# Kernel tuning notes

Measured on AMD Instinct MI355X. Metric: run time of the kernel, lower is better.

The kernel has to match this reference:

```python
import jax, jax.numpy as jnp
import numpy as np

B, S, H, C = 16, 64, 1024, 16


def setup_inputs() -> dict:
    key = jax.random.key(0)
    ks = jax.random.split(key, 14)
    sH = 1.0 / np.sqrt(H)
    # binary strictly-lower-triangular ancestor mask (DAG adjacency)
    dep = (jax.random.uniform(ks[0], (B, S, S)) < 0.3).astype(jnp.float32)
    dep = dep * jnp.tril(jnp.ones((S, S), jnp.float32), k=-1)[None]
    node_encoding = jax.random.normal(ks[1], (B, S, C), jnp.float32)
    u = lambda k, shape: jax.random.uniform(k, shape, jnp.float32, -sH, sH)
    return {
        'dep_graph': dep,
        'node_encoding': node_encoding,
        'gate_w': u(ks[2], (H, H)), 'gate_b': u(ks[3], (H,)),
        'map_w': u(ks[4], (H, H)), 'map_b': u(ks[5], (H,)),
        'w_ih': u(ks[6], (3 * H, C)), 'w_hh': u(ks[7], (3 * H, H)),
        'b_ih': u(ks[8], (3 * H,)), 'b_hh': u(ks[9], (3 * H,)),
        'lin11_w': u(ks[10], (H, H)), 'lin11_b': u(ks[11], (H,)),
        'lin12_w': u(ks[12], (H, H)), 'lin12_b': u(ks[13], (H,)),
    }


def reference(dep_graph, node_encoding, gate_w, gate_b, map_w, map_b,
              w_ih, w_hh, b_ih, b_hh, lin11_w, lin11_b, lin12_w, lin12_b):
    Bv, Sv, _ = dep_graph.shape
    Hv = gate_w.shape[0]

    def gru_cell(x, h):  # PyTorch GRUCell semantics, gate order r,z,n
        gi = x @ w_ih.T + b_ih
        gh = h @ w_hh.T + b_hh
        ir, iz, inn = jnp.split(gi, 3, axis=-1)
        hr, hz, hn = jnp.split(gh, 3, axis=-1)
        r = jax.nn.sigmoid(ir + hr)
        z = jax.nn.sigmoid(iz + hz)
        n = jnp.tanh(inn + r * hn)
        return (1.0 - z) * n + z * h

    def step(state, inp):  # state: [B,S,H]
        mask, x, t = inp  # mask [B,S], x [B,C]
        masked = state * mask[:, :, None]  # [B,S,H]
        g = jax.nn.sigmoid(jnp.einsum('bsh,oh->bso', masked, gate_w) + gate_b)
        m = jnp.einsum('bsh,oh->bso', masked, map_w) + map_b
        h_in = jnp.sum(g * m, axis=1)  # [B,H]
        hv = gru_cell(x, h_in)
        return state.at[:, t].set(hv), hv

    init = jnp.zeros((Bv, Sv, Hv), dep_graph.dtype)
    xs = (jnp.swapaxes(dep_graph, 0, 1),
          jnp.swapaxes(node_encoding, 0, 1),
          jnp.arange(Sv))
    _, hvs = jax.lax.scan(step, init, xs)
    hv = hvs[-1]  # [B,H]
    mu = hv @ lin11_w.T + lin11_b
    logvar = hv @ lin12_w.T + lin12_b
    return hv, mu, logvar
```

## Files before the change

kernel.cpp:

```cpp
#include <hip/hip_runtime.h>


#define NT 512
#define NBLK 256

typedef unsigned int uint;
typedef __attribute__((ext_vector_type(2))) _Float16 half2v;
typedef __attribute__((ext_vector_type(2))) uint uint2v;
typedef __attribute__((ext_vector_type(4))) uint uint4v;
typedef __attribute__((ext_vector_type(4))) int int4v;

__device__ __forceinline__ float fdot2(uint w, uint h, float acc) {
#if __has_builtin(__builtin_amdgcn_fdot2)
    return __builtin_amdgcn_fdot2(__builtin_bit_cast(half2v, w),
                                  __builtin_bit_cast(half2v, h), acc, false);
#else
    half2v a = __builtin_bit_cast(half2v, w);
    half2v b = __builtin_bit_cast(half2v, h);
    return acc + (float)a[0] * (float)b[0] + (float)a[1] * (float)b[1];
#endif
}

__device__ __forceinline__ uint packh2(float a, float b) {
    half2v h; h[0] = (_Float16)a; h[1] = (_Float16)b;
    return __builtin_bit_cast(uint, h);
}

__device__ __forceinline__ float sigm(float x) { return 1.0f / (1.0f + __expf(-x)); }
__device__ __forceinline__ float tanhfast(float x) { return 2.0f / (1.0f + __expf(-2.0f * x)) - 1.0f; }

__device__ __forceinline__ void stage4(const uint* src, uint* lds, int tid) {
    const uint* a0 = src + tid * 4;
    const uint* a1 = a0 + 2048;
    const uint* a2 = a0 + 4096;
    const uint* a3 = a0 + 6144;
    uint4v u0, u1, u2, u3;
    asm volatile("global_load_dwordx4 %0, %4, off sc0 sc1\n\t"
                 "global_load_dwordx4 %1, %5, off sc0 sc1\n\t"
                 "global_load_dwordx4 %2, %6, off sc0 sc1\n\t"
                 "global_load_dwordx4 %3, %7, off sc0 sc1\n\t"
                 "s_waitcnt vmcnt(0)"
                 : "=&v"(u0), "=&v"(u1), "=&v"(u2), "=&v"(u3)
                 : "v"(a0), "v"(a1), "v"(a2), "v"(a3) : "memory");
    *(uint4v*)(lds + tid * 4)        = u0;
    *(uint4v*)(lds + tid * 4 + 2048) = u1;
    *(uint4v*)(lds + tid * 4 + 4096) = u2;
    *(uint4v*)(lds + tid * 4 + 6144) = u3;
}

__device__ __forceinline__ void st_dev2_wait(uint* p, uint lo, uint hi) {
    uint2v v; v[0] = lo; v[1] = hi;
    asm volatile("global_store_dwordx2 %0, %1, off sc0 sc1\n\ts_waitcnt vmcnt(0)"
                 :: "v"(p), "v"(v) : "memory");
}
__device__ __forceinline__ void st_flag_noack(int* p, int v) {
    asm volatile("global_store_dword %0, %1, off sc0 sc1" :: "v"(p), "v"(v) : "memory");
}

__device__ __forceinline__ void wait_flags(const int* fl, int gen) {
    if (threadIdx.x < 64) {
        const int* pp = fl + threadIdx.x * 4;
        bool done;
        do {
            int4v v;
            asm volatile("global_load_dwordx4 %0, %1, off sc0 sc1\n\ts_waitcnt vmcnt(0)"
                         : "=v"(v) : "v"(pp) : "memory");
            done = __all(v[0] >= gen && v[1] >= gen && v[2] >= gen && v[3] >= gen);
        } while (!done);
    }
    __syncthreads();
}

__device__ __forceinline__ void loadw4(uint* arr, const float* rowk) {
    float4 a = ((const float4*)rowk)[0];
    float4 b = ((const float4*)rowk)[1];
    arr[0] = packh2(a.x, a.y);
    arr[1] = packh2(a.z, a.w);
    arr[2] = packh2(b.x, b.y);
    arr[3] = packh2(b.z, b.w);
}

__device__ __forceinline__ void rscat16(float (&a)[16], bool h32, bool h16, bool h8, bool h4b) {
#pragma unroll
    for (int j = 0; j < 8; j++) {
        float snd = h32 ? a[j] : a[j + 8];
        float kp  = h32 ? a[j + 8] : a[j];
        a[j] = kp + __shfl_xor(snd, 32, 64);
    }
#pragma unroll
    for (int j = 0; j < 4; j++) {
        float snd = h16 ? a[j] : a[j + 4];
        float kp  = h16 ? a[j + 4] : a[j];
        a[j] = kp + __shfl_xor(snd, 16, 64);
    }
#pragma unroll
    for (int j = 0; j < 2; j++) {
        float snd = h8 ? a[j] : a[j + 2];
        float kp  = h8 ? a[j + 2] : a[j];
        a[j] = kp + __shfl_xor(snd, 8, 64);
    }
    {
        float snd = h4b ? a[0] : a[1];
        float kp  = h4b ? a[1] : a[0];
        a[0] = kp + __shfl_xor(snd, 4, 64);
    }
}

__global__ __launch_bounds__(NT) void enc_kernel(
    const float* __restrict__ dep, const float* __restrict__ ne,
    const float* __restrict__ gate_w, const float* __restrict__ gate_b,
    const float* __restrict__ map_w, const float* __restrict__ map_b,
    const float* __restrict__ w_ih, const float* __restrict__ w_hh,
    const float* __restrict__ b_ih, const float* __restrict__ b_hh,
    int* __restrict__ flags, uint* __restrict__ hv_ex, uint* __restrict__ hin_ex,
    float* __restrict__ out)
{
    __shared__ __align__(16) uint shm[20416];
    uint*  hvS   = shm;
    float* GM    = (float*)(shm + 8192);
    float* red   = (float*)(shm + 16512);
    float* hbuf  = (float*)(shm + 18048);
    float* hbuf2 = (float*)(shm + 18112);
    float* wihb  = (float*)(shm + 18176);
    uint*  depb  = shm + 18368;

    const int tid  = threadIdx.x;
    const int bid  = blockIdx.x;
    const int o0   = bid * 4;
    const int w    = tid >> 6;
    const int lane = tid & 63;
    const bool h32 = (lane & 32) != 0, h16 = (lane & 16) != 0;
    const bool h8  = (lane & 8) != 0,  h4b = (lane & 4) != 0;
    const int olw  = lane & 3;
    const int kseg = w * 16 + (lane >> 2);
    const int k0   = kseg * 8;

    uint wG[4], wM[4], wR[4], wZ[4], wN[4];
    loadw4(wG, gate_w + (o0 + olw) * 1024 + k0);
    loadw4(wM, map_w + (o0 + olw) * 1024 + k0);
    loadw4(wR, w_hh + (o0 + olw) * 1024 + k0);
    loadw4(wZ, w_hh + (1024 + o0 + olw) * 1024 + k0);
    loadw4(wN, w_hh + (2048 + o0 + olw) * 1024 + k0);

#pragma unroll
    for (int e = 0; e < 4; e++) {
        int idx = tid + e * 512;
        int b = idx >> 7, tt = (idx >> 1) & 63, hf = idx & 1;
        const float4* dp = (const float4*)(dep + ((b * 64 + tt) * 64) + hf * 32);
        uint bits = 0;
#pragma unroll
        for (int s4 = 0; s4 < 8; s4++) {
            float4 v = dp[s4];
            bits |= (v.x != 0.0f) ? (1u << (s4 * 4 + 0)) : 0u;
            bits |= (v.y != 0.0f) ? (1u << (s4 * 4 + 1)) : 0u;
            bits |= (v.z != 0.0f) ? (1u << (s4 * 4 + 2)) : 0u;
            bits |= (v.w != 0.0f) ? (1u << (s4 * 4 + 3)) : 0u;
        }
        depb[idx] = bits;
    }
    if (tid < 192) {
        int g = tid >> 6, ol = (tid >> 4) & 3, c = tid & 15;
        wihb[tid] = w_ih[(g * 1024 + o0 + ol) * 16 + c];
    }

    const int prS = tid >> 3;
    const int bS = prS >> 2, olS = prS & 3, soct = tid & 7;
    const float gbS = gate_b[o0 + olS];
    const float mbS = map_b[o0 + olS];
    const float baseS = sigm(gbS) * mbS;
    const int bP = tid >> 2, olP = tid & 3, oP = o0 + olP;
    const float gbP = gate_b[oP], mbP = map_b[oP];
    const float basP = sigm(gbP) * mbP;
    const float bir = b_ih[oP], biz = b_ih[1024 + oP], bin_ = b_ih[2048 + oP];
    const float bhr = b_hh[oP], bhz = b_hh[1024 + oP], bhn = b_hh[2048 + oP];
    __syncthreads();

    for (int t = 0; t < 64; t++) {
        {
            uint bl = depb[bS * 128 + t * 2 + (soct >> 2)];
            uint bits8 = (bl >> ((soct & 3) * 8)) & 0xFFu;
            int s0 = soct * 8;
            const float* Gp = GM + prS * 65;
            const float* Mp = GM + 4160 + prS * 65;
            float part = 0.0f;
#pragma unroll
            for (int j = 0; j < 8; j++) {
                int s = s0 + j;
                float Gv = Gp[s], Mv = Mp[s];
                float term = ((bits8 >> j) & 1u) ? (sigm(Gv + gbS) * (Mv + mbS)) : baseS;
                part += (s == t - 1) ? 0.0f : term;
            }
            part += __shfl_xor(part, 1, 64);
            part += __shfl_xor(part, 2, 64);
            part += __shfl_xor(part, 4, 64);
            if (soct == 0) hbuf2[prS] = part;
        }

        if (t > 0) {
            wait_flags(flags, 2 * t);
            stage4(hv_ex, hvS, tid);
            __syncthreads();
            float aG[16], aM[16];
#pragma unroll
            for (int b = 0; b < 16; b++) { aG[b] = 0.0f; aM[b] = 0.0f; }
#pragma unroll
            for (int b = 0; b < 16; b++) {
                uint4v hq = *(const uint4v*)&hvS[b * 512 + kseg * 4];
#pragma unroll
                for (int q = 0; q < 4; q++) {
                    aG[b] = fdot2(wG[q], hq[q], aG[b]);
                    aM[b] = fdot2(wM[q], hq[q], aM[b]);
                }
            }
            rscat16(aG, h32, h16, h8, h4b);
            rscat16(aM, h32, h16, h8, h4b);
            red[w * 64 + lane]       = aG[0];
            red[512 + w * 64 + lane] = aM[0];
            __syncthreads();
            if (tid < 64) {
                float nG = 0.0f, nM = 0.0f;
#pragma unroll
                for (int ww = 0; ww < 8; ww++) {
                    nG += red[ww * 64 + tid];
                    nM += red[512 + ww * 64 + tid];
                }
                GM[tid * 65 + (t - 1)] = nG;
                GM[4160 + tid * 65 + (t - 1)] = nM;
                uint blb = depb[bP * 128 + t * 2 + ((t - 1) >> 5)];
                int bit = (blb >> ((t - 1) & 31)) & 1;
                float term = bit ? (sigm(nG + gbP) * (nM + mbP)) : basP;
                hbuf[tid] = hbuf2[tid] + term;
            }
        } else {
            __syncthreads();
            if (tid < 64) hbuf[tid] = hbuf2[tid];
        }
        __syncthreads();
        if (tid < 16) {
            uint p0 = packh2(hbuf[tid * 4 + 0], hbuf[tid * 4 + 1]);
            uint p1 = packh2(hbuf[tid * 4 + 2], hbuf[tid * 4 + 3]);
            st_dev2_wait(hin_ex + tid * 512 + bid * 2, p0, p1);
        }
        __syncthreads();
        if (tid == 0) st_flag_noack(flags + bid, 2 * t + 1);

        float gi0 = 0.0f, gi1 = 0.0f, gi2 = 0.0f;
        if (tid < 64) {
            const float* xr = ne + (bP * 64 + t) * 16;
            float4 xa = ((const float4*)xr)[0];
            float4 xb = ((const float4*)xr)[1];
            float4 xc = ((const float4*)xr)[2];
            float4 xd = ((const float4*)xr)[3];
            const float4* w0p = (const float4*)&wihb[olP * 16];
            const float4* w1p = (const float4*)&wihb[64 + olP * 16];
            const float4* w2p = (const float4*)&wihb[128 + olP * 16];
            float4 a0 = w0p[0], a1 = w0p[1], a2 = w0p[2], a3 = w0p[3];
            gi0 = a0.x*xa.x + a0.y*xa.y + a0.z*xa.z + a0.w*xa.w
                + a1.x*xb.x + a1.y*xb.y + a1.z*xb.z + a1.w*xb.w
                + a2.x*xc.x + a2.y*xc.y + a2.z*xc.z + a2.w*xc.w
                + a3.x*xd.x + a3.y*xd.y + a3.z*xd.z + a3.w*xd.w;
            float4 b0 = w1p[0], b1 = w1p[1], b2 = w1p[2], b3 = w1p[3];
            gi1 = b0.x*xa.x + b0.y*xa.y + b0.z*xa.z + b0.w*xa.w
                + b1.x*xb.x + b1.y*xb.y + b1.z*xb.z + b1.w*xb.w
                + b2.x*xc.x + b2.y*xc.y + b2.z*xc.z + b2.w*xc.w
                + b3.x*xd.x + b3.y*xd.y + b3.z*xd.z + b3.w*xd.w;
            float4 c0 = w2p[0], c1 = w2p[1], c2 = w2p[2], c3 = w2p[3];
            gi2 = c0.x*xa.x + c0.y*xa.y + c0.z*xa.z + c0.w*xa.w
                + c1.x*xb.x + c1.y*xb.y + c1.z*xb.z + c1.w*xb.w
                + c2.x*xc.x + c2.y*xc.y + c2.z*xc.z + c2.w*xc.w
                + c3.x*xd.x + c3.y*xd.y + c3.z*xd.z + c3.w*xd.w;
        }
        wait_flags(flags, 2 * t + 1);
        stage4(hin_ex, hvS, tid);
        __syncthreads();
        float aR[16], aZ[16], aN[16];
#pragma unroll
        for (int b = 0; b < 16; b++) { aR[b] = 0.0f; aZ[b] = 0.0f; aN[b] = 0.0f; }
#pragma unroll
        for (int b = 0; b < 16; b++) {
            uint4v hq = *(const uint4v*)&hvS[b * 512 + kseg * 4];
#pragma unroll
            for (int q = 0; q < 4; q++) {
                aR[b] = fdot2(wR[q], hq[q], aR[b]);
                aZ[b] = fdot2(wZ[q], hq[q], aZ[b]);
                aN[b] = fdot2(wN[q], hq[q], aN[b]);
            }
        }
        rscat16(aR, h32, h16, h8, h4b);
        rscat16(aZ, h32, h16, h8, h4b);
        rscat16(aN, h32, h16, h8, h4b);
        red[w * 64 + lane]        = aR[0];
        red[512 + w * 64 + lane]  = aZ[0];
        red[1024 + w * 64 + lane] = aN[0];
        __syncthreads();
        if (tid < 64) {
            float ghr = 0.0f, ghz = 0.0f, ghn = 0.0f;
#pragma unroll
            for (int ww = 0; ww < 8; ww++) {
                ghr += red[ww * 64 + tid];
                ghz += red[512 + ww * 64 + tid];
                ghn += red[1024 + ww * 64 + tid];
            }
            float h_in = hbuf[tid];
            float r = sigm(gi0 + bir + ghr + bhr);
            float z = sigm(gi1 + biz + ghz + bhz);
            float n = tanhfast(gi2 + bin_ + r * (ghn + bhn));
            float hv = (1.0f - z) * n + z * h_in;
            if (t == 63) out[bP * 1024 + oP] = hv;
            hbuf[tid] = hv;
        }
        __syncthreads();
        if (t < 63) {
            if (tid < 16) {
                uint p0 = packh2(hbuf[tid * 4 + 0], hbuf[tid * 4 + 1]);
                uint p1 = packh2(hbuf[tid * 4 + 2], hbuf[tid * 4 + 3]);
                st_dev2_wait(hv_ex + tid * 512 + bid * 2, p0, p1);
            }
            __syncthreads();
            if (tid == 0) st_flag_noack(flags + bid, 2 * t + 2);
        }
    }
}

__device__ __forceinline__ float wave_sum(float v) {
    v += __shfl_xor(v, 32, 64);
    v += __shfl_xor(v, 16, 64);
    v += __shfl_xor(v, 8, 64);
    v += __shfl_xor(v, 4, 64);
    v += __shfl_xor(v, 2, 64);
    v += __shfl_xor(v, 1, 64);
    return v;
}

__global__ __launch_bounds__(256) void kF(
    float* out, const float* __restrict__ w1, const float* __restrict__ b1,
    const float* __restrict__ w2, const float* __restrict__ b2)
{
    const int wid = threadIdx.x >> 6;
    const int kl = threadIdx.x & 63;
    const int o = blockIdx.x * 2 + (wid >> 1);
    const int b0 = (wid & 1) * 8;

    float w1v[16], w2v[16];
#pragma unroll
    for (int i = 0; i < 16; i++) {
        w1v[i] = w1[o * 1024 + kl + 64 * i];
        w2v[i] = w2[o * 1024 + kl + 64 * i];
    }
    for (int b = b0; b < b0 + 8; b++) {
        float p1 = 0.0f, p2 = 0.0f;
#pragma unroll
        for (int i = 0; i < 16; i++) {
            float h = out[b * 1024 + kl + 64 * i];
            p1 += h * w1v[i];
            p2 += h * w2v[i];
        }
        p1 = wave_sum(p1);
        p2 = wave_sum(p2);
        if (kl == 0) {
            out[16384 + b * 1024 + o] = p1 + b1[o];
            out[32768 + b * 1024 + o] = p2 + b2[o];
        }
    }
}

extern "C" void kernel_launch(void* const* d_in, const int* in_sizes, int n_in,
                              void* d_out, int out_size, void* d_ws, size_t ws_size,
                              hipStream_t stream) {
    const float* dep     = (const float*)d_in[0];
    const float* ne      = (const float*)d_in[1];
    const float* gate_w  = (const float*)d_in[2];
    const float* gate_b  = (const float*)d_in[3];
    const float* map_w   = (const float*)d_in[4];
    const float* map_b   = (const float*)d_in[5];
    const float* w_ih    = (const float*)d_in[6];
    const float* w_hh    = (const float*)d_in[7];
    const float* b_ih    = (const float*)d_in[8];
    const float* b_hh    = (const float*)d_in[9];
    const float* lin11_w = (const float*)d_in[10];
    const float* lin11_b = (const float*)d_in[11];
    const float* lin12_w = (const float*)d_in[12];
    const float* lin12_b = (const float*)d_in[13];

    int* wsI = (int*)d_ws;
    int* flags   = wsI;
    uint* hv_ex  = (uint*)(wsI + 256);
    uint* hin_ex = hv_ex + 8192;
    float* outp  = (float*)d_out;

    hipMemsetAsync((void*)flags, 0, 256 * 4, stream);

    void* args[] = {
        (void*)&dep, (void*)&ne, (void*)&gate_w, (void*)&gate_b,
        (void*)&map_w, (void*)&map_b, (void*)&w_ih, (void*)&w_hh,
        (void*)&b_ih, (void*)&b_hh,
        (void*)&flags, (void*)&hv_ex, (void*)&hin_ex, (void*)&outp,
    };
    hipError_t e = hipLaunchCooperativeKernel((void*)enc_kernel, dim3(NBLK), dim3(NT),
                                              args, 0, stream);
    if (e != hipSuccess) {
        enc_kernel<<<dim3(NBLK), dim3(NT), 0, stream>>>(
            dep, ne, gate_w, gate_b, map_w, map_b, w_ih, w_hh, b_ih, b_hh,
            flags, hv_ex, hin_ex, outp);
    }
    kF<<<dim3(512), dim3(256), 0, stream>>>(outp, lin11_w, lin11_b, lin12_w, lin12_b);
}
```

Baseline: 574.9 us.

## Split batch into two groups with separate flags to overlap grid exchanges

```diff
diff --git a/kernel.cpp b/kernel.cpp
--- a/kernel.cpp
+++ b/kernel.cpp
@@ -29,23 +29,16 @@
 __device__ __forceinline__ float sigm(float x) { return 1.0f / (1.0f + __expf(-x)); }
 __device__ __forceinline__ float tanhfast(float x) { return 2.0f / (1.0f + __expf(-2.0f * x)) - 1.0f; }
 
-__device__ __forceinline__ void stage4(const uint* src, uint* lds, int tid) {
+__device__ __forceinline__ void stage2(const uint* src, uint* lds, int tid) {
     const uint* a0 = src + tid * 4;
     const uint* a1 = a0 + 2048;
-    const uint* a2 = a0 + 4096;
-    const uint* a3 = a0 + 6144;
-    uint4v u0, u1, u2, u3;
-    asm volatile("global_load_dwordx4 %0, %4, off sc0 sc1\n\t"
-                 "global_load_dwordx4 %1, %5, off sc0 sc1\n\t"
-                 "global_load_dwordx4 %2, %6, off sc0 sc1\n\t"
-                 "global_load_dwordx4 %3, %7, off sc0 sc1\n\t"
+    uint4v u0, u1;
+    asm volatile("global_load_dwordx4 %0, %2, off sc0 sc1\n\t"
+                 "global_load_dwordx4 %1, %3, off sc0 sc1\n\t"
                  "s_waitcnt vmcnt(0)"
-                 : "=&v"(u0), "=&v"(u1), "=&v"(u2), "=&v"(u3)
-                 : "v"(a0), "v"(a1), "v"(a2), "v"(a3) : "memory");
+                 : "=&v"(u0), "=&v"(u1) : "v"(a0), "v"(a1) : "memory");
     *(uint4v*)(lds + tid * 4)        = u0;
     *(uint4v*)(lds + tid * 4 + 2048) = u1;
-    *(uint4v*)(lds + tid * 4 + 4096) = u2;
-    *(uint4v*)(lds + tid * 4 + 6144) = u3;
 }
 
 __device__ __forceinline__ void st_dev2_wait(uint* p, uint lo, uint hi) {
@@ -80,30 +73,25 @@
     arr[3] = packh2(b.z, b.w);
 }
 
-__device__ __forceinline__ void rscat16(float (&a)[16], bool h32, bool h16, bool h8, bool h4b) {
-#pragma unroll
-    for (int j = 0; j < 8; j++) {
-        float snd = h32 ? a[j] : a[j + 8];
-        float kp  = h32 ? a[j + 8] : a[j];
+__device__ __forceinline__ void rscat8(float (&a)[8], bool h32, bool h16, bool h8) {
+#pragma unroll
+    for (int j = 0; j < 4; j++) {
+        float snd = h32 ? a[j] : a[j + 4];
+        float kp  = h32 ? a[j + 4] : a[j];
         a[j] = kp + __shfl_xor(snd, 32, 64);
     }
 #pragma unroll
-    for (int j = 0; j < 4; j++) {
-        float snd = h16 ? a[j] : a[j + 4];
-        float kp  = h16 ? a[j + 4] : a[j];
+    for (int j = 0; j < 2; j++) {
+        float snd = h16 ? a[j] : a[j + 2];
+        float kp  = h16 ? a[j + 2] : a[j];
         a[j] = kp + __shfl_xor(snd, 16, 64);
     }
-#pragma unroll
-    for (int j = 0; j < 2; j++) {
-        float snd = h8 ? a[j] : a[j + 2];
-        float kp  = h8 ? a[j + 2] : a[j];
-        a[j] = kp + __shfl_xor(snd, 8, 64);
-    }
     {
-        float snd = h4b ? a[0] : a[1];
-        float kp  = h4b ? a[1] : a[0];
-        a[0] = kp + __shfl_xor(snd, 4, 64);
-    }
+        float snd = h8 ? a[0] : a[1];
+        float kp  = h8 ? a[1] : a[0];
+        a[0] = kp + __shfl_xor(snd, 8, 64);
+    }
+    a[0] += __shfl_xor(a[0], 4, 64);
 }
 
 __global__ __launch_bounds__(NT) void enc_kernel(
@@ -115,22 +103,22 @@
     int* __restrict__ flags, uint* __restrict__ hv_ex, uint* __restrict__ hin_ex,
     float* __restrict__ out)
 {
-    __shared__ __align__(16) uint shm[20416];
+    __shared__ __align__(16) uint shm[16512];
     uint*  hvS   = shm;
-    float* GM    = (float*)(shm + 8192);
-    float* red   = (float*)(shm + 16512);
-    float* hbuf  = (float*)(shm + 18048);
-    float* hbuf2 = (float*)(shm + 18112);
-    float* wihb  = (float*)(shm + 18176);
-    uint*  depb  = shm + 18368;
+    float* GM    = (float*)(shm + 4096);
+    float* red   = (float*)(shm + 12416);
+    float* hbuf  = (float*)(shm + 13952);
+    float* hbuf2 = (float*)(shm + 14016);
+    float* gibuf = (float*)(shm + 14080);
+    float* wihb  = (float*)(shm + 14272);
+    uint*  depb  = shm + 14464;
 
     const int tid  = threadIdx.x;
     const int bid  = blockIdx.x;
     const int o0   = bid * 4;
     const int w    = tid >> 6;
     const int lane = tid & 63;
-    const bool h32 = (lane & 32) != 0, h16 = (lane & 16) != 0;
-    const bool h8  = (lane & 8) != 0,  h4b = (lane & 4) != 0;
+    const bool h32 = (lane & 32) != 0, h16 = (lane & 16) != 0, h8 = (lane & 8) != 0;
     const int olw  = lane & 3;
     const int kseg = w * 16 + (lane >> 2);
     const int k0   = kseg * 8;
@@ -168,14 +156,34 @@
     const float gbS = gate_b[o0 + olS];
     const float mbS = map_b[o0 + olS];
     const float baseS = sigm(gbS) * mbS;
-    const int bP = tid >> 2, olP = tid & 3, oP = o0 + olP;
-    const float gbP = gate_b[oP], mbP = map_b[oP];
-    const float basP = sigm(gbP) * mbP;
-    const float bir = b_ih[oP], biz = b_ih[1024 + oP], bin_ = b_ih[2048 + oP];
-    const float bhr = b_hh[oP], bhz = b_hh[1024 + oP], bhn = b_hh[2048 + oP];
+    const int olQ = tid & 3, oQ = o0 + olQ, blQ = tid >> 2;
+    const float gbQ = gate_b[oQ], mbQ = map_b[oQ];
+    const float basQ = sigm(gbQ) * mbQ;
+    const float bir = b_ih[oQ], biz = b_ih[1024 + oQ], bin_ = b_ih[2048 + oQ];
+    const float bhr = b_hh[oQ], bhz = b_hh[1024 + oQ], bhn = b_hh[2048 + oQ];
     __syncthreads();
 
+    int* fgA[2] = { flags, flags + 256 };
+
     for (int t = 0; t < 64; t++) {
+        if (tid < 64) {
+            int bg = tid >> 2;
+            const float* xr = ne + (bg * 64 + t) * 16;
+            float4 xa = ((const float4*)xr)[0];
+            float4 xb = ((const float4*)xr)[1];
+            float4 xc = ((const float4*)xr)[2];
+            float4 xd = ((const float4*)xr)[3];
+#pragma unroll
+            for (int g3 = 0; g3 < 3; g3++) {
+                const float4* wp = (const float4*)&wihb[(g3 * 4 + olQ) * 16];
+                float4 a0 = wp[0], a1 = wp[1], a2 = wp[2], a3 = wp[3];
+                gibuf[g3 * 64 + tid] =
+                      a0.x*xa.x + a0.y*xa.y + a0.z*xa.z + a0.w*xa.w
+                    + a1.x*xb.x + a1.y*xb.y + a1.z*xb.z + a1.w*xb.w
+                    + a2.x*xc.x + a2.y*xc.y + a2.z*xc.z + a2.w*xc.w
+                    + a3.x*xd.x + a3.y*xd.y + a3.z*xd.z + a3.w*xd.w;
+            }
+        }
         {
             uint bl = depb[bS * 128 + t * 2 + (soct >> 2)];
             uint bits8 = (bl >> ((soct & 3) * 8)) & 0xFFu;
@@ -195,129 +203,115 @@
             part += __shfl_xor(part, 4, 64);
             if (soct == 0) hbuf2[prS] = part;
         }
-
-        if (t > 0) {
-            wait_flags(flags, 2 * t);
-            stage4(hv_ex, hvS, tid);
+        __syncthreads();
+
+#pragma unroll
+        for (int g = 0; g < 2; g++) {
+            int*  fg   = fgA[g];
+            uint* hvx  = hv_ex  + g * 4096;
+            uint* hinx = hin_ex + g * 4096;
+            if (t > 0) {
+                wait_flags(fg, 2 * t);
+                stage2(hvx, hvS, tid);
+                __syncthreads();
+                float aG[8], aM[8];
+#pragma unroll
+                for (int b = 0; b < 8; b++) { aG[b] = 0.0f; aM[b] = 0.0f; }
+#pragma unroll
+                for (int b = 0; b < 8; b++) {
+                    uint4v hq = *(const uint4v*)&hvS[b * 512 + kseg * 4];
+#pragma unroll
+                    for (int q = 0; q < 4; q++) {
+                        aG[b] = fdot2(wG[q], hq[q], aG[b]);
+                        aM[b] = fdot2(wM[q], hq[q], aM[b]);
+                    }
+                }
+                rscat8(aG, h32, h16, h8);
+                rscat8(aM, h32, h16, h8);
+                red[w * 64 + lane]       = aG[0];
+                red[512 + w * 64 + lane] = aM[0];
+                __syncthreads();
+                if (tid < 32) {
+                    int rl = (blQ << 3) | olQ;
+                    float nG = 0.0f, nM = 0.0f;
+#pragma unroll
+                    for (int ww = 0; ww < 8; ww++) {
+                        nG += red[ww * 64 + rl];
+                        nM += red[512 + ww * 64 + rl];
+                    }
+                    int pair = g * 32 + tid;
+                    GM[pair * 65 + (t - 1)] = nG;
+                    GM[4160 + pair * 65 + (t - 1)] = nM;
+                    uint blb = depb[(g * 8 + blQ) * 128 + t * 2 + ((t - 1) >> 5)];
+                    int bit = (blb >> ((t - 1) & 31)) & 1;
+                    float term = bit ? (sigm(nG + gbQ) * (nM + mbQ)) : basQ;
+                    hbuf[pair] = hbuf2[pair] + term;
+                }
+            } else {
+                if (tid < 32) hbuf[g * 32 + tid] = hbuf2[g * 32 + tid];
+            }
+            if (tid < 8) {
+                uint p0 = packh2(hbuf[g * 32 + tid * 4 + 0], hbuf[g * 32 + tid * 4 + 1]);
+                uint p1 = packh2(hbuf[g * 32 + tid * 4 + 2], hbuf[g * 32 + tid * 4 + 3]);
+                st_dev2_wait(hinx + tid * 512 + bid * 2, p0, p1);
+            }
+            if (tid == 0) st_flag_noack(fg + bid, 2 * t + 1);
+        }
+
+#pragma unroll
+        for (int g = 0; g < 2; g++) {
+            int*  fg   = fgA[g];
+            uint* hvx  = hv_ex  + g * 4096;
+            uint* hinx = hin_ex + g * 4096;
+            wait_flags(fg, 2 * t + 1);
+            stage2(hinx, hvS, tid);
             __syncthreads();
-            float aG[16], aM[16];
-#pragma unroll
-            for (int b = 0; b < 16; b++) { aG[b] = 0.0f; aM[b] = 0.0f; }
-#pragma unroll
-            for (int b = 0; b < 16; b++) {
+            float aR[8], aZ[8], aN[8];
+#pragma unroll
+            for (int b = 0; b < 8; b++) { aR[b] = 0.0f; aZ[b] = 0.0f; aN[b] = 0.0f; }
+#pragma unroll
+            for (int b = 0; b < 8; b++) {
                 uint4v hq = *(const uint4v*)&hvS[b * 512 + kseg * 4];
 #pragma unroll
                 for (int q = 0; q < 4; q++) {
-                    aG[b] = fdot2(wG[q], hq[q], aG[b]);
-                    aM[b] = fdot2(wM[q], hq[q], aM[b]);
+                    aR[b] = fdot2(wR[q], hq[q], aR[b]);
+                    aZ[b] = fdot2(wZ[q], hq[q], aZ[b]);
+                    aN[b] = fdot2(wN[q], hq[q], aN[b]);
                 }
             }
-            rscat16(aG, h32, h16, h8, h4b);
-            rscat16(aM, h32, h16, h8, h4b);
-            red[w * 64 + lane]       = aG[0];
-            red[512 + w * 64 + lane] = aM[0];
+            rscat8(aR, h32, h16, h8);
+            rscat8(aZ, h32, h16, h8);
+            rscat8(aN, h32, h16, h8);
+            red[w * 64 + lane]        = aR[0];
+            red[512 + w * 64 + lane]  = aZ[0];
+            red[1024 + w * 64 + lane] = aN[0];
             __syncthreads();
-            if (tid < 64) {
-                float nG = 0.0f, nM = 0.0f;
+            if (tid < 32) {
+                int rl = (blQ << 3) | olQ;
+                float ghr = 0.0f, ghz = 0.0f, ghn = 0.0f;
 #pragma unroll
                 for (int ww = 0; ww < 8; ww++) {
-                    nG += red[ww * 64 + tid];
-                    nM += red[512 + ww * 64 + tid];
+                    ghr += red[ww * 64 + rl];
+                    ghz += red[512 + ww * 64 + rl];
+                    ghn += red[1024 + ww * 64 + rl];
                 }
-                GM[tid * 65 + (t - 1)] = nG;
-                GM[4160 + tid * 65 + (t - 1)] = nM;
-                uint blb = depb[bP * 128 + t * 2 + ((t - 1) >> 5)];
-                int bit = (blb >> ((t - 1) & 31)) & 1;
-                float term = bit ? (sigm(nG + gbP) * (nM + mbP)) : basP;
-                hbuf[tid] = hbuf2[tid] + term;
-            }
-        } else {
-            __syncthreads();
-            if (tid < 64) hbuf[tid] = hbuf2[tid];
-        }
-        __syncthreads();
-        if (tid < 16) {
-            uint p0 = packh2(hbuf[tid * 4 + 0], hbuf[tid * 4 + 1]);
-            uint p1 = packh2(hbuf[tid * 4 + 2], hbuf[tid * 4 + 3]);
-            st_dev2_wait(hin_ex + tid * 512 + bid * 2, p0, p1);
-        }
-        __syncthreads();
-        if (tid == 0) st_flag_noack(flags + bid, 2 * t + 1);
-
-        float gi0 = 0.0f, gi1 = 0.0f, gi2 = 0.0f;
-        if (tid < 64) {
-            const float* xr = ne + (bP * 64 + t) * 16;
-            float4 xa = ((const float4*)xr)[0];
-            float4 xb = ((const float4*)xr)[1];
-            float4 xc = ((const float4*)xr)[2];
-            float4 xd = ((const float4*)xr)[3];
-            const float4* w0p = (const float4*)&wihb[olP * 16];
-            const float4* w1p = (const float4*)&wihb[64 + olP * 16];
-            const float4* w2p = (const float4*)&wihb[128 + olP * 16];
-            float4 a0 = w0p[0], a1 = w0p[1], a2 = w0p[2], a3 = w0p[3];
-            gi0 = a0.x*xa.x + a0.y*xa.y + a0.z*xa.z + a0.w*xa.w
-                + a1.x*xb.x + a1.y*xb.y + a1.z*xb.z + a1.w*xb.w
-                + a2.x*xc.x + a2.y*xc.y + a2.z*xc.z + a2.w*xc.w
-                + a3.x*xd.x + a3.y*xd.y + a3.z*xd.z + a3.w*xd.w;
-            float4 b0 = w1p[0], b1 = w1p[1], b2 = w1p[2], b3 = w1p[3];
-            gi1 = b0.x*xa.x + b0.y*xa.y + b0.z*xa.z + b0.w*xa.w
-                + b1.x*xb.x + b1.y*xb.y + b1.z*xb.z + b1.w*xb.w
-                + b2.x*xc.x + b2.y*xc.y + b2.z*xc.z + b2.w*xc.w
-                + b3.x*xd.x + b3.y*xd.y + b3.z*xd.z + b3.w*xd.w;
-            float4 c0 = w2p[0], c1 = w2p[1], c2 = w2p[2], c3 = w2p[3];
-            gi2 = c0.x*xa.x + c0.y*xa.y + c0.z*xa.z + c0.w*xa.w
-                + c1.x*xb.x + c1.y*xb.y + c1.z*xb.z + c1.w*xb.w
-                + c2.x*xc.x + c2.y*xc.y + c2.z*xc.z + c2.w*xc.w
-                + c3.x*xd.x + c3.y*xd.y + c3.z*xd.z + c3.w*xd.w;
-        }
-        wait_flags(flags, 2 * t + 1);
-        stage4(hin_ex, hvS, tid);
-        __syncthreads();
-        float aR[16], aZ[16], aN[16];
-#pragma unroll
-        for (int b = 0; b < 16; b++) { aR[b] = 0.0f; aZ[b] = 0.0f; aN[b] = 0.0f; }
-#pragma unroll
-        for (int b = 0; b < 16; b++) {
-            uint4v hq = *(const uint4v*)&hvS[b * 512 + kseg * 4];
-#pragma unroll
-            for (int q = 0; q < 4; q++) {
-                aR[b] = fdot2(wR[q], hq[q], aR[b]);
-                aZ[b] = fdot2(wZ[q], hq[q], aZ[b]);
-                aN[b] = fdot2(wN[q], hq[q], aN[b]);
-            }
-        }
-        rscat16(aR, h32, h16, h8, h4b);
-        rscat16(aZ, h32, h16, h8, h4b);
-        rscat16(aN, h32, h16, h8, h4b);
-        red[w * 64 + lane]        = aR[0];
-        red[512 + w * 64 + lane]  = aZ[0];
-        red[1024 + w * 64 + lane] = aN[0];
-        __syncthreads();
-        if (tid < 64) {
-            float ghr = 0.0f, ghz = 0.0f, ghn = 0.0f;
-#pragma unroll
-            for (int ww = 0; ww < 8; ww++) {
-                ghr += red[ww * 64 + tid];
-                ghz += red[512 + ww * 64 + tid];
-                ghn += red[1024 + ww * 64 + tid];
-            }
-            float h_in = hbuf[tid];
-            float r = sigm(gi0 + bir + ghr + bhr);
-            float z = sigm(gi1 + biz + ghz + bhz);
-            float n = tanhfast(gi2 + bin_ + r * (ghn + bhn));
-            float hv = (1.0f - z) * n + z * h_in;
-            if (t == 63) out[bP * 1024 + oP] = hv;
-            hbuf[tid] = hv;
-        }
-        __syncthreads();
-        if (t < 63) {
-            if (tid < 16) {
-                uint p0 = packh2(hbuf[tid * 4 + 0], hbuf[tid * 4 + 1]);
-                uint p1 = packh2(hbuf[tid * 4 + 2], hbuf[tid * 4 + 3]);
-                st_dev2_wait(hv_ex + tid * 512 + bid * 2, p0, p1);
-            }
-            __syncthreads();
-            if (tid == 0) st_flag_noack(flags + bid, 2 * t + 2);
+                int pair = g * 32 + tid;
+                float h_in = hbuf[pair];
+                float r = sigm(gibuf[pair] + bir + ghr + bhr);
+                float z = sigm(gibuf[64 + pair] + biz + ghz + bhz);
+                float n = tanhfast(gibuf[128 + pair] + bin_ + r * (ghn + bhn));
+                float hv = (1.0f - z) * n + z * h_in;
+                if (t == 63) out[(g * 8 + blQ) * 1024 + oQ] = hv;
+                hbuf[pair] = hv;
+            }
+            if (t < 63) {
+                if (tid < 8) {
+                    uint p0 = packh2(hbuf[g * 32 + tid * 4 + 0], hbuf[g * 32 + tid * 4 + 1]);
+                    uint p1 = packh2(hbuf[g * 32 + tid * 4 + 2], hbuf[g * 32 + tid * 4 + 3]);
+                    st_dev2_wait(hvx + tid * 512 + bid * 2, p0, p1);
+                }
+                if (tid == 0) st_flag_noack(fg + bid, 2 * t + 2);
+            }
         }
     }
 }
@@ -384,11 +378,11 @@
 
     int* wsI = (int*)d_ws;
     int* flags   = wsI;
-    uint* hv_ex  = (uint*)(wsI + 256);
+    uint* hv_ex  = (uint*)(wsI + 512);
     uint* hin_ex = hv_ex + 8192;
     float* outp  = (float*)d_out;
 
-    hipMemsetAsync((void*)flags, 0, 256 * 4, stream);
+    hipMemsetAsync((void*)flags, 0, 512 * 4, stream);
 
     void* args[] = {
         (void*)&dep, (void*)&ne, (void*)&gate_w, (void*)&gate_b,
```

After: 722.5 us. +25.7%, slower.

## Replace flag-based grid barriers with parity-tagged data polling

Applied to the files above, without the earlier changes.

```diff
diff --git a/kernel.cpp b/kernel.cpp
--- a/kernel.cpp
+++ b/kernel.cpp
@@ -8,7 +8,6 @@
 typedef __attribute__((ext_vector_type(2))) _Float16 half2v;
 typedef __attribute__((ext_vector_type(2))) uint uint2v;
 typedef __attribute__((ext_vector_type(4))) uint uint4v;
-typedef __attribute__((ext_vector_type(4))) int int4v;
 
 __device__ __forceinline__ float fdot2(uint w, uint h, float acc) {
 #if __has_builtin(__builtin_amdgcn_fdot2)
@@ -29,46 +28,37 @@
 __device__ __forceinline__ float sigm(float x) { return 1.0f / (1.0f + __expf(-x)); }
 __device__ __forceinline__ float tanhfast(float x) { return 2.0f / (1.0f + __expf(-2.0f * x)) - 1.0f; }
 
-__device__ __forceinline__ void stage4(const uint* src, uint* lds, int tid) {
+__device__ __forceinline__ void pollstage4(const uint* src, uint* lds, int tid, uint want) {
     const uint* a0 = src + tid * 4;
     const uint* a1 = a0 + 2048;
     const uint* a2 = a0 + 4096;
     const uint* a3 = a0 + 6144;
     uint4v u0, u1, u2, u3;
-    asm volatile("global_load_dwordx4 %0, %4, off sc0 sc1\n\t"
-                 "global_load_dwordx4 %1, %5, off sc0 sc1\n\t"
-                 "global_load_dwordx4 %2, %6, off sc0 sc1\n\t"
-                 "global_load_dwordx4 %3, %7, off sc0 sc1\n\t"
-                 "s_waitcnt vmcnt(0)"
-                 : "=&v"(u0), "=&v"(u1), "=&v"(u2), "=&v"(u3)
-                 : "v"(a0), "v"(a1), "v"(a2), "v"(a3) : "memory");
+    for (;;) {
+        asm volatile("global_load_dwordx4 %0, %4, off sc0 sc1\n\t"
+                     "global_load_dwordx4 %1, %5, off sc0 sc1\n\t"
+                     "global_load_dwordx4 %2, %6, off sc0 sc1\n\t"
+                     "global_load_dwordx4 %3, %7, off sc0 sc1\n\t"
+                     "s_waitcnt vmcnt(0)"
+                     : "=&v"(u0), "=&v"(u1), "=&v"(u2), "=&v"(u3)
+                     : "v"(a0), "v"(a1), "v"(a2), "v"(a3) : "memory");
+        uint andv = u0[0] & u0[1] & u0[2] & u0[3] & u1[0] & u1[1] & u1[2] & u1[3]
+                  & u2[0] & u2[1] & u2[2] & u2[3] & u3[0] & u3[1] & u3[2] & u3[3];
+        uint orv  = u0[0] | u0[1] | u0[2] | u0[3] | u1[0] | u1[1] | u1[2] | u1[3]
+                  | u2[0] | u2[1] | u2[2] | u2[3] | u3[0] | u3[1] | u3[2] | u3[3];
+        if (want ? ((andv & 1u) != 0u) : ((orv & 1u) == 0u)) break;
+    }
     *(uint4v*)(lds + tid * 4)        = u0;
     *(uint4v*)(lds + tid * 4 + 2048) = u1;
     *(uint4v*)(lds + tid * 4 + 4096) = u2;
     *(uint4v*)(lds + tid * 4 + 6144) = u3;
 }
 
-__device__ __forceinline__ void st_dev2_wait(uint* p, uint lo, uint hi) {
-    uint2v v; v[0] = lo; v[1] = hi;
-    asm volatile("global_store_dwordx2 %0, %1, off sc0 sc1\n\ts_waitcnt vmcnt(0)"
-                 :: "v"(p), "v"(v) : "memory");
-}
-__device__ __forceinline__ void st_flag_noack(int* p, int v) {
-    asm volatile("global_store_dword %0, %1, off sc0 sc1" :: "v"(p), "v"(v) : "memory");
-}
-
-__device__ __forceinline__ void wait_flags(const int* fl, int gen) {
-    if (threadIdx.x < 64) {
-        const int* pp = fl + threadIdx.x * 4;
-        bool done;
-        do {
-            int4v v;
-            asm volatile("global_load_dwordx4 %0, %1, off sc0 sc1\n\ts_waitcnt vmcnt(0)"
-                         : "=v"(v) : "v"(pp) : "memory");
-            done = __all(v[0] >= gen && v[1] >= gen && v[2] >= gen && v[3] >= gen);
-        } while (!done);
-    }
-    __syncthreads();
+__device__ __forceinline__ void st_pub2(uint* p, uint lo, uint hi, uint tag) {
+    uint2v v;
+    v[0] = (lo & ~1u) | tag;
+    v[1] = (hi & ~1u) | tag;
+    asm volatile("global_store_dwordx2 %0, %1, off sc0 sc1" :: "v"(p), "v"(v) : "memory");
 }
 
 __device__ __forceinline__ void loadw4(uint* arr, const float* rowk) {
@@ -112,7 +102,7 @@
     const float* __restrict__ map_w, const float* __restrict__ map_b,
     const float* __restrict__ w_ih, const float* __restrict__ w_hh,
     const float* __restrict__ b_ih, const float* __restrict__ b_hh,
-    int* __restrict__ flags, uint* __restrict__ hv_ex, uint* __restrict__ hin_ex,
+    uint* __restrict__ hv_ex, uint* __restrict__ hin_ex,
     float* __restrict__ out)
 {
     __shared__ __align__(16) uint shm[20416];
@@ -176,6 +166,7 @@
     __syncthreads();
 
     for (int t = 0; t < 64; t++) {
+        const uint tagT = (uint)(t & 1);
         {
             uint bl = depb[bS * 128 + t * 2 + (soct >> 2)];
             uint bits8 = (bl >> ((soct & 3) * 8)) & 0xFFu;
@@ -197,8 +188,7 @@
         }
 
         if (t > 0) {
-            wait_flags(flags, 2 * t);
-            stage4(hv_ex, hvS, tid);
+            pollstage4(hv_ex, hvS, tid, tagT ^ 1u);
             __syncthreads();
             float aG[16], aM[16];
 #pragma unroll
@@ -239,10 +229,8 @@
         if (tid < 16) {
             uint p0 = packh2(hbuf[tid * 4 + 0], hbuf[tid * 4 + 1]);
             uint p1 = packh2(hbuf[tid * 4 + 2], hbuf[tid * 4 + 3]);
-            st_dev2_wait(hin_ex + tid * 512 + bid * 2, p0, p1);
-        }
-        __syncthreads();
-        if (tid == 0) st_flag_noack(flags + bid, 2 * t + 1);
+            st_pub2(hin_ex + tid * 512 + bid * 2, p0, p1, tagT);
+        }
 
         float gi0 = 0.0f, gi1 = 0.0f, gi2 = 0.0f;
         if (tid < 64) {
@@ -270,8 +258,7 @@
                 + c2.x*xc.x + c2.y*xc.y + c2.z*xc.z + c2.w*xc.w
                 + c3.x*xd.x + c3.y*xd.y + c3.z*xd.z + c3.w*xd.w;
         }
-        wait_flags(flags, 2 * t + 1);
-        stage4(hin_ex, hvS, tid);
+        pollstage4(hin_ex, hvS, tid, tagT);
         __syncthreads();
         float aR[16], aZ[16], aN[16];
 #pragma unroll
@@ -310,14 +297,10 @@
             hbuf[tid] = hv;
         }
         __syncthreads();
-        if (t < 63) {
-            if (tid < 16) {
-                uint p0 = packh2(hbuf[tid * 4 + 0], hbuf[tid * 4 + 1]);
-                uint p1 = packh2(hbuf[tid * 4 + 2], hbuf[tid * 4 + 3]);
-                st_dev2_wait(hv_ex + tid * 512 + bid * 2, p0, p1);
-            }
-            __syncthreads();
-            if (tid == 0) st_flag_noack(flags + bid, 2 * t + 2);
+        if (t < 63 && tid < 16) {
+            uint p0 = packh2(hbuf[tid * 4 + 0], hbuf[tid * 4 + 1]);
+            uint p1 = packh2(hbuf[tid * 4 + 2], hbuf[tid * 4 + 3]);
+            st_pub2(hv_ex + tid * 512 + bid * 2, p0, p1, tagT);
         }
     }
 }
@@ -382,26 +365,24 @@
     const float* lin12_w = (const float*)d_in[12];
     const float* lin12_b = (const float*)d_in[13];
 
-    int* wsI = (int*)d_ws;
-    int* flags   = wsI;
-    uint* hv_ex  = (uint*)(wsI + 256);
+    uint* hv_ex  = (uint*)d_ws;
     uint* hin_ex = hv_ex + 8192;
     float* outp  = (float*)d_out;
 
-    hipMemsetAsync((void*)flags, 0, 256 * 4, stream);
+    hipMemsetAsync((void*)hv_ex, 0xFF, 2 * 8192 * 4, stream);
 
     void* args[] = {
         (void*)&dep, (void*)&ne, (void*)&gate_w, (void*)&gate_b,
         (void*)&map_w, (void*)&map_b, (void*)&w_ih, (void*)&w_hh,
         (void*)&b_ih, (void*)&b_hh,
-        (void*)&flags, (void*)&hv_ex, (void*)&hin_ex, (void*)&outp,
+        (void*)&hv_ex, (void*)&hin_ex, (void*)&outp,
     };
     hipError_t e = hipLaunchCooperativeKernel((void*)enc_kernel, dim3(NBLK), dim3(NT),
                                               args, 0, stream);
     if (e != hipSuccess) {
         enc_kernel<<<dim3(NBLK), dim3(NT), 0, stream>>>(
             dep, ne, gate_w, gate_b, map_w, map_b, w_ih, w_hh, b_ih, b_hh,
-            flags, hv_ex, hin_ex, outp);
+            hv_ex, hin_ex, outp);
     }
     kF<<<dim3(512), dim3(256), 0, stream>>>(outp, lin11_w, lin11_b, lin12_w, lin12_b);
 }
```

After: 637.2 us. 10.8% more time.

## Tag exchanged fp16 data with step parity to drop store-ack waits

Applied to the files above, without the earlier changes.

```diff
diff --git a/kernel.cpp b/kernel.cpp
--- a/kernel.cpp
+++ b/kernel.cpp
@@ -29,29 +29,37 @@
 __device__ __forceinline__ float sigm(float x) { return 1.0f / (1.0f + __expf(-x)); }
 __device__ __forceinline__ float tanhfast(float x) { return 2.0f / (1.0f + __expf(-2.0f * x)) - 1.0f; }
 
-__device__ __forceinline__ void stage4(const uint* src, uint* lds, int tid) {
+__device__ __forceinline__ void stagev4(const uint* src, uint* lds, int tid, uint want) {
     const uint* a0 = src + tid * 4;
     const uint* a1 = a0 + 2048;
     const uint* a2 = a0 + 4096;
     const uint* a3 = a0 + 6144;
     uint4v u0, u1, u2, u3;
-    asm volatile("global_load_dwordx4 %0, %4, off sc0 sc1\n\t"
-                 "global_load_dwordx4 %1, %5, off sc0 sc1\n\t"
-                 "global_load_dwordx4 %2, %6, off sc0 sc1\n\t"
-                 "global_load_dwordx4 %3, %7, off sc0 sc1\n\t"
-                 "s_waitcnt vmcnt(0)"
-                 : "=&v"(u0), "=&v"(u1), "=&v"(u2), "=&v"(u3)
-                 : "v"(a0), "v"(a1), "v"(a2), "v"(a3) : "memory");
+    for (;;) {
+        asm volatile("global_load_dwordx4 %0, %4, off sc0 sc1\n\t"
+                     "global_load_dwordx4 %1, %5, off sc0 sc1\n\t"
+                     "global_load_dwordx4 %2, %6, off sc0 sc1\n\t"
+                     "global_load_dwordx4 %3, %7, off sc0 sc1\n\t"
+                     "s_waitcnt vmcnt(0)"
+                     : "=&v"(u0), "=&v"(u1), "=&v"(u2), "=&v"(u3)
+                     : "v"(a0), "v"(a1), "v"(a2), "v"(a3) : "memory");
+        uint andv = u0[0] & u0[1] & u0[2] & u0[3] & u1[0] & u1[1] & u1[2] & u1[3]
+                  & u2[0] & u2[1] & u2[2] & u2[3] & u3[0] & u3[1] & u3[2] & u3[3];
+        uint orv  = u0[0] | u0[1] | u0[2] | u0[3] | u1[0] | u1[1] | u1[2] | u1[3]
+                  | u2[0] | u2[1] | u2[2] | u2[3] | u3[0] | u3[1] | u3[2] | u3[3];
+        if (want ? ((andv & 1u) != 0u) : ((orv & 1u) == 0u)) break;
+    }
     *(uint4v*)(lds + tid * 4)        = u0;
     *(uint4v*)(lds + tid * 4 + 2048) = u1;
     *(uint4v*)(lds + tid * 4 + 4096) = u2;
     *(uint4v*)(lds + tid * 4 + 6144) = u3;
 }
 
-__device__ __forceinline__ void st_dev2_wait(uint* p, uint lo, uint hi) {
-    uint2v v; v[0] = lo; v[1] = hi;
-    asm volatile("global_store_dwordx2 %0, %1, off sc0 sc1\n\ts_waitcnt vmcnt(0)"
-                 :: "v"(p), "v"(v) : "memory");
+__device__ __forceinline__ void st_pub2(uint* p, uint lo, uint hi, uint tag) {
+    uint2v v;
+    v[0] = (lo & ~1u) | tag;
+    v[1] = (hi & ~1u) | tag;
+    asm volatile("global_store_dwordx2 %0, %1, off sc0 sc1" :: "v"(p), "v"(v) : "memory");
 }
 __device__ __forceinline__ void st_flag_noack(int* p, int v) {
     asm volatile("global_store_dword %0, %1, off sc0 sc1" :: "v"(p), "v"(v) : "memory");
@@ -176,6 +184,7 @@
     __syncthreads();
 
     for (int t = 0; t < 64; t++) {
+        const uint tagT = (uint)(t & 1);
         {
             uint bl = depb[bS * 128 + t * 2 + (soct >> 2)];
             uint bits8 = (bl >> ((soct & 3) * 8)) & 0xFFu;
@@ -198,7 +207,7 @@
 
         if (t > 0) {
             wait_flags(flags, 2 * t);
-            stage4(hv_ex, hvS, tid);
+            stagev4(hv_ex, hvS, tid, tagT ^ 1u);
             __syncthreads();
             float aG[16], aM[16];
 #pragma unroll
@@ -235,13 +244,11 @@
             __syncthreads();
             if (tid < 64) hbuf[tid] = hbuf2[tid];
         }
-        __syncthreads();
         if (tid < 16) {
             uint p0 = packh2(hbuf[tid * 4 + 0], hbuf[tid * 4 + 1]);
             uint p1 = packh2(hbuf[tid * 4 + 2], hbuf[tid * 4 + 3]);
-            st_dev2_wait(hin_ex + tid * 512 + bid * 2, p0, p1);
-        }
-        __syncthreads();
+            st_pub2(hin_ex + tid * 512 + bid * 2, p0, p1, tagT);
+        }
         if (tid == 0) st_flag_noack(flags + bid, 2 * t + 1);
 
         float gi0 = 0.0f, gi1 = 0.0f, gi2 = 0.0f;
@@ -271,7 +278,7 @@
                 + c3.x*xd.x + c3.y*xd.y + c3.z*xd.z + c3.w*xd.w;
         }
         wait_flags(flags, 2 * t + 1);
-        stage4(hin_ex, hvS, tid);
+        stagev4(hin_ex, hvS, tid, tagT);
         __syncthreads();
         float aR[16], aZ[16], aN[16];
 #pragma unroll
@@ -309,16 +316,15 @@
             if (t == 63) out[bP * 1024 + oP] = hv;
             hbuf[tid] = hv;
         }
-        __syncthreads();
         if (t < 63) {
             if (tid < 16) {
                 uint p0 = packh2(hbuf[tid * 4 + 0], hbuf[tid * 4 + 1]);
                 uint p1 = packh2(hbuf[tid * 4 + 2], hbuf[tid * 4 + 3]);
-                st_dev2_wait(hv_ex + tid * 512 + bid * 2, p0, p1);
-            }
-            __syncthreads();
+                st_pub2(hv_ex + tid * 512 + bid * 2, p0, p1, tagT);
+            }
             if (tid == 0) st_flag_noack(flags + bid, 2 * t + 2);
         }
+        __syncthreads();
     }
 }
 
@@ -389,6 +395,7 @@
     float* outp  = (float*)d_out;
 
     hipMemsetAsync((void*)flags, 0, 256 * 4, stream);
+    hipMemsetAsync((void*)hv_ex, 0xFF, 2 * 8192 * 4, stream);
 
     void* args[] = {
         (void*)&dep, (void*)&ne, (void*)&gate_w, (void*)&gate_b,
```

Measured after the change: 528.5 us (median of 2 runs). 1.09x faster.
